# Performance work log

Hardware: AMD Instinct MI355X
Metric: run time of the kernel (lower is better)

The kernel has to match this reference:

```python
import jax, jax.numpy as jnp
import numpy as np

EPS = 1e-12  # torch F.normalize eps
RBF_SCALE = 10.0


def _l2norm(x, axis=-1):
    n = jnp.sqrt(jnp.sum(x * x, axis=axis, keepdims=True))
    return x / jnp.maximum(n, EPS)


def setup_inputs() -> dict:
    key = jax.random.key(0)
    k1, k2, k3 = jax.random.split(key, 3)
    N, D, C = 32768, 1024, 2048
    inp = jax.random.normal(k1, (N, D), dtype=jnp.float32)
    pos = jax.random.normal(k2, (C, D), dtype=jnp.float32)
    # offset is initialized to zeros in torch; use small random values so the
    # output is non-trivial for kernel correctness testing.
    offset = 0.01 * jax.random.normal(k3, (C, D), dtype=jnp.float32)
    return {"inp": inp, "pos": pos, "offset": offset}


def reference(inp, pos, offset):
    a = _l2norm(inp)                       # [N, D]
    b = _l2norm(pos)                       # [C, D]
    dist = 1.0 - jnp.einsum('nd,cd->nc', a, b)   # [N, C] cosine distance
    w = jnp.exp(-RBF_SCALE * dist)               # RBF cluster weights
    # The torch for-loop  out += offset[i] * dist[:, i, None]  is a GEMM:
    out = inp + jnp.einsum('nc,cd->nd', w, offset)
    out = _l2norm(out)
    offset_reg = jnp.sum(offset * offset)
    return (out, offset_reg)
```

## Files before the change

kernel.cpp:

```cpp
#include <hip/hip_runtime.h>

typedef float  f32x4  __attribute__((ext_vector_type(4)));
typedef float  f32x16 __attribute__((ext_vector_type(16)));
typedef int    i32x4  __attribute__((ext_vector_type(4)));
typedef int    i32x8  __attribute__((ext_vector_type(8)));

__device__ __forceinline__ unsigned int f2e4m3(float x){
    union{float f; unsigned u;} v; v.f = x;
    unsigned s = (v.u >> 24) & 0x80u;
    float ax = fabsf(x);
    if (ax > 448.0f) ax = 448.0f;
    if (ax < 0.015625f){
        int d = (int)__builtin_rintf(ax * 512.0f);
        return s | (unsigned)d;
    }
    v.f = ax;
    unsigned u = v.u + 0x7ffffu + ((v.u >> 20) & 1u);
    unsigned E = (u >> 23) - 120u;
    unsigned M = (u >> 20) & 7u;
    return s | (E << 3) | M;
}

__device__ __forceinline__ unsigned int pk4(float x0, float x1, float x2, float x3){
#if __has_builtin(__builtin_amdgcn_cvt_pk_fp8_f32)
    int u = __builtin_amdgcn_cvt_pk_fp8_f32(x0, x1, 0, false);
    u     = __builtin_amdgcn_cvt_pk_fp8_f32(x2, x3, u, true);
    return (unsigned)u;
#else
    return f2e4m3(x0) | (f2e4m3(x1) << 8) | (f2e4m3(x2) << 16) | (f2e4m3(x3) << 24);
#endif
}

__device__ __forceinline__ i32x8 ld_frag(const char* p0, const char* p1){
    i32x4 lo = *(const i32x4*)p0;
    i32x4 hi = *(const i32x4*)p1;
    return __builtin_shufflevector(lo, hi, 0,1,2,3,4,5,6,7);
}


__global__ __launch_bounds__(256) void norm_rows_fp8(const float* __restrict__ in,
                                                     unsigned char* __restrict__ out){
    const int row = blockIdx.x;
    const int t   = threadIdx.x;
    f32x4 x = ((const f32x4*)(in + (size_t)row * 1024))[t];
    float ss = x[0]*x[0] + x[1]*x[1] + x[2]*x[2] + x[3]*x[3];
    #pragma unroll
    for (int o = 32; o > 0; o >>= 1) ss += __shfl_xor(ss, o);
    __shared__ float red[4];
    if ((t & 63) == 0) red[t >> 6] = ss;
    __syncthreads();
    float tot = red[0] + red[1] + red[2] + red[3];
    float inv = 16.0f / fmaxf(sqrtf(tot), 1e-12f);
    unsigned u = pk4(x[0]*inv, x[1]*inv, x[2]*inv, x[3]*inv);
    size_t addr = ((size_t)(row >> 5) * 16 + (t >> 4)) * 2048
                + (size_t)((t >> 3) & 1) * 1024
                + (size_t)(row & 31) * 32 + ((4 * t) & 31);
    *(unsigned int*)(out + addr) = u;
}

__global__ __launch_bounds__(256) void norm_rows_f32(float* __restrict__ buf){
    const int row = blockIdx.x;
    const int t   = threadIdx.x;
    f32x4* p = (f32x4*)(buf + (size_t)row * 1024);
    f32x4 x = p[t];
    float ss = x[0]*x[0] + x[1]*x[1] + x[2]*x[2] + x[3]*x[3];
    #pragma unroll
    for (int o = 32; o > 0; o >>= 1) ss += __shfl_xor(ss, o);
    __shared__ float red[4];
    if ((t & 63) == 0) red[t >> 6] = ss;
    __syncthreads();
    float tot = red[0] + red[1] + red[2] + red[3];
    float inv = 1.0f / fmaxf(sqrtf(tot), 1e-12f);
    p[t] = x * inv;
}

__global__ __launch_bounds__(256) void transpose_off(const float* __restrict__ off,
                                                     unsigned char* __restrict__ offt,
                                                     float* __restrict__ reg_out){
    __shared__ unsigned char t_lds[64][68];
    const int t  = threadIdx.x;
    const int c0 = blockIdx.x * 64;
    const int d0 = blockIdx.y * 64;
    float ss = 0.f;
    #pragma unroll
    for (int p = 0; p < 4; ++p){
        int c  = p * 16 + (t >> 4);
        int dq = t & 15;
        f32x4 v = *(const f32x4*)(off + (size_t)(c0 + c) * 1024 + d0 + dq * 4);
        ss += v[0]*v[0] + v[1]*v[1] + v[2]*v[2] + v[3]*v[3];
        unsigned u = pk4(v[0]*64.0f, v[1]*64.0f, v[2]*64.0f, v[3]*64.0f);
        #pragma unroll
        for (int j = 0; j < 4; ++j) t_lds[dq * 4 + j][c] = (unsigned char)(u >> (8*j));
    }
    __syncthreads();
    #pragma unroll
    for (int i = 0; i < 4; ++i){
        int byte_o = (t + 256 * i) * 4;
        int fs  = byte_o >> 11;
        int rem = byte_o & 2047;
        int dl  = fs * 32 + ((rem >> 5) & 31);
        int cl  = ((rem >> 10) & 1) * 32 + (rem & 31);
        unsigned int v = *(const unsigned int*)&t_lds[dl][cl];
        size_t f = (size_t)((d0 >> 5) + fs);
        *(unsigned int*)(offt + (f * 32 + (c0 >> 6)) * 2048 + rem) = v;
    }
    #pragma unroll
    for (int o = 32; o > 0; o >>= 1) ss += __shfl_xor(ss, o);
    __shared__ float red[4];
    if ((t & 63) == 0) red[t >> 6] = ss;
    __syncthreads();
    if (t == 0) atomicAdd(reg_out, red[0] + red[1] + red[2] + red[3]);
}

template<int EPI, int SA, int SB, int NT>
__global__ __launch_bounds__(256, 2)
void gemm_fl(const unsigned char* __restrict__ A,
             const unsigned char* __restrict__ B,
             unsigned char* __restrict__ Wout, int wNT,
             const float* __restrict__ Cadd,
             float* __restrict__ Fout, int ldo)
{
    const int tid = threadIdx.x;

    int bx = blockIdx.x, by = blockIdx.y;
    {
        const int gx = gridDim.x, gy = gridDim.y;
        const int nwg = gx * gy;
        if ((nwg & 7) == 0){
            const int lid = bx + gx * by;
            const int q   = nwg >> 3;
            const int n   = (lid & 7) * q + (lid >> 3);
            const int sh  = 31 - __clz(gy);
            bx = n >> sh;
            by = n & (gy - 1);
        }
    }
    const int m0  = bx * 256;
    const int n0  = by * 128;
    const int wid = tid >> 6, lane = tid & 63;
    const int wr  = wid >> 1, wc = wid & 1;
    const int l31 = lane & 31, hg = lane >> 5;

    const char* pA[4];
    const char* pB[2];
    #pragma unroll
    for (int m = 0; m < 4; ++m)
        pA[m] = (const char*)A
              + ((size_t)((m0 + wr * 128 + m * 32) >> 5) * NT) * 2048 + lane * 32;
    #pragma unroll
    for (int n = 0; n < 2; ++n)
        pB[n] = (const char*)B
              + ((size_t)((n0 + wc * 64 + n * 32) >> 5) * NT) * 2048 + lane * 32;

    f32x16 acc[4][2] = {};
    i32x8 a0[4], b0[2], a1[4], b1[2];

    #pragma unroll
    for (int m = 0; m < 4; ++m) a0[m] = ld_frag(pA[m], pA[m] + 16);
    #pragma unroll
    for (int n = 0; n < 2; ++n) b0[n] = ld_frag(pB[n], pB[n] + 16);

#define MFMA8(av, bv) { __builtin_amdgcn_s_setprio(1); \
    _Pragma("unroll") for (int mi = 0; mi < 4; ++mi) \
    _Pragma("unroll") for (int ni = 0; ni < 2; ++ni) \
        acc[mi][ni] = __builtin_amdgcn_mfma_scale_f32_32x32x64_f8f6f4( \
            av[mi], bv[ni], acc[mi][ni], 0, 0, 0, SA, 0, SB); \
    __builtin_amdgcn_s_setprio(0); }

    #pragma unroll 1
    for (int t = 0; t < NT; t += 2){
        const size_t o1 = (size_t)(t + 1) * 2048;
        #pragma unroll
        for (int m = 0; m < 4; ++m) a1[m] = ld_frag(pA[m] + o1, pA[m] + o1 + 16);
        #pragma unroll
        for (int n = 0; n < 2; ++n) b1[n] = ld_frag(pB[n] + o1, pB[n] + o1 + 16);
        MFMA8(a0, b0);
        const size_t o2 = (size_t)(t + 2 < NT ? t + 2 : NT - 1) * 2048;
        #pragma unroll
        for (int m = 0; m < 4; ++m) a0[m] = ld_frag(pA[m] + o2, pA[m] + o2 + 16);
        #pragma unroll
        for (int n = 0; n < 2; ++n) b0[n] = ld_frag(pB[n] + o2, pB[n] + o2 + 16);
        MFMA8(a1, b1);
    }
#undef MFMA8

    asm volatile("s_nop 7\n\ts_nop 7");

    if (EPI == 1){
        const int tq = (n0 + wc * 64) >> 6;
        #pragma unroll
        for (int m = 0; m < 4; ++m){
            const size_t fW = (size_t)((m0 + wr * 128 + m * 32) >> 5);
            #pragma unroll
            for (int n = 0; n < 2; ++n){
                unsigned char* base = Wout + (fW * wNT + tq) * 2048
                                    + (size_t)n * 1024 + l31;
                #pragma unroll
                for (int q = 0; q < 4; ++q){
                    float w0 = exp2f(fmaf(14.4269504f, acc[m][n][4*q+0], -4.4269504f));
                    float w1 = exp2f(fmaf(14.4269504f, acc[m][n][4*q+1], -4.4269504f));
                    float w2 = exp2f(fmaf(14.4269504f, acc[m][n][4*q+2], -4.4269504f));
                    float w3 = exp2f(fmaf(14.4269504f, acc[m][n][4*q+3], -4.4269504f));
                    unsigned u = pk4(w0, w1, w2, w3);
                    unsigned char* p = base + (size_t)(8 * q + 4 * hg) * 32;
                    p[0]  = (unsigned char)u;
                    p[32] = (unsigned char)(u >> 8);
                    p[64] = (unsigned char)(u >> 16);
                    p[96] = (unsigned char)(u >> 24);
                }
            }
        }
    } else {
        #pragma unroll
        for (int m = 0; m < 4; ++m){
            #pragma unroll
            for (int n = 0; n < 2; ++n){
                const int grb = m0 + wr * 128 + m * 32;
                const int gc  = n0 + wc * 64 + n * 32 + l31;
                #pragma unroll
                for (int r = 0; r < 16; ++r){
                    const int row = (r & 3) + 8 * (r >> 2) + 4 * hg;
                    Fout[(size_t)(grb + row) * ldo + gc] =
                        Cadd[(size_t)(grb + row) * ldo + gc] + acc[m][n][r];
                }
            }
        }
    }
}

extern "C" void kernel_launch(void* const* d_in, const int* in_sizes, int n_in,
                              void* d_out, int out_size, void* d_ws, size_t ws_size,
                              hipStream_t stream)
{
    (void)n_in; (void)out_size;
    const float* inp = (const float*)d_in[0];
    const float* pos = (const float*)d_in[1];
    const float* off = (const float*)d_in[2];
    float* out = (float*)d_out;

    const int D = 1024, C = 2048;
    const int N = in_sizes[0] / D;

    unsigned char* b_fp8 = (unsigned char*)d_ws;
    unsigned char* offt  = b_fp8 + (size_t)C * D;
    unsigned char* a_fp8 = offt + (size_t)D * C;
    size_t fixed = (size_t)C * D * 2;
    size_t avail = ws_size > fixed ? ws_size - fixed : 0;
    int Mc = 256;
    for (int cand = N; cand >= 256; cand >>= 1){
        if ((size_t)cand * (size_t)(D + C) <= avail){ Mc = cand; break; }
    }
    if (Mc > N) Mc = N;
    unsigned char* w_buf = a_fp8 + (size_t)Mc * D;

    float* reg_out = out + (size_t)N * D;
    hipMemsetAsync(reg_out, 0, sizeof(float), stream);

    transpose_off<<<dim3(C / 64, D / 64), 256, 0, stream>>>(off, offt, reg_out);
    norm_rows_fp8<<<C, 256, 0, stream>>>(pos, b_fp8);

    for (int r0 = 0; r0 < N; r0 += Mc){
        norm_rows_fp8<<<Mc, 256, 0, stream>>>(inp + (size_t)r0 * D, a_fp8);
        gemm_fl<1,123,123,16><<<dim3(Mc / 256, C / 128), 256, 0, stream>>>(
            a_fp8, b_fp8, w_buf, C / 64, nullptr, nullptr, 0);
        gemm_fl<2,117,121,32><<<dim3(Mc / 256, D / 128), 256, 0, stream>>>(
            w_buf, offt, nullptr, 0, inp + (size_t)r0 * D, out + (size_t)r0 * D, D);
    }
    norm_rows_f32<<<N, 256, 0, stream>>>(out);
}
```

Baseline: 279.4 us.

## Stage A tiles through LDS with async global-to-LDS loads in 256x256 blocks

Replaces the register-only fp8 GEMM with a hybrid kernel that streams the row-major A operand into a triple-buffered, swizzled LDS ring using global_load_lds. B fragments are still loaded straight from global in the pre-tiled layout. The block tile grows to 256x256 with 512 threads, so A data is shared across more waves and fewer blocks re-read it. The activations and the weight buffer now use a plain row-major layout. This adds a barrier on every K step and 48KB of LDS per block, and the W epilogue still does scattered byte stores.

```diff
diff --git a/kernel.cpp b/kernel.cpp
--- a/kernel.cpp
+++ b/kernel.cpp
@@ -4,6 +4,9 @@
 typedef float  f32x16 __attribute__((ext_vector_type(16)));
 typedef int    i32x4  __attribute__((ext_vector_type(4)));
 typedef int    i32x8  __attribute__((ext_vector_type(8)));
+
+#define AS1 __attribute__((address_space(1)))
+#define AS3 __attribute__((address_space(3)))
 
 __device__ __forceinline__ unsigned int f2e4m3(float x){
     union{float f; unsigned u;} v; v.f = x;
@@ -31,15 +34,38 @@
 #endif
 }
 
+__device__ __forceinline__ void gload16(const unsigned char* g, const char* l){
+    __builtin_amdgcn_global_load_lds((const AS1 void*)g, (AS3 void*)l, 16, 0, 0);
+}
+
 __device__ __forceinline__ i32x8 ld_frag(const char* p0, const char* p1){
     i32x4 lo = *(const i32x4*)p0;
     i32x4 hi = *(const i32x4*)p1;
     return __builtin_shufflevector(lo, hi, 0,1,2,3,4,5,6,7);
 }
 
-
-__global__ __launch_bounds__(256) void norm_rows_fp8(const float* __restrict__ in,
-                                                     unsigned char* __restrict__ out){
+#define GBAR() do{ asm volatile("" ::: "memory"); __builtin_amdgcn_s_barrier(); \
+                   asm volatile("" ::: "memory"); }while(0)
+#define VMW(N)  asm volatile("s_waitcnt vmcnt(" #N ")" ::: "memory")
+
+__global__ __launch_bounds__(256) void norm_rows_fp8_rm(const float* __restrict__ in,
+                                                        unsigned int* __restrict__ out){
+    const int row = blockIdx.x;
+    const int t   = threadIdx.x;
+    f32x4 x = ((const f32x4*)(in + (size_t)row * 1024))[t];
+    float ss = x[0]*x[0] + x[1]*x[1] + x[2]*x[2] + x[3]*x[3];
+    #pragma unroll
+    for (int o = 32; o > 0; o >>= 1) ss += __shfl_xor(ss, o);
+    __shared__ float red[4];
+    if ((t & 63) == 0) red[t >> 6] = ss;
+    __syncthreads();
+    float tot = red[0] + red[1] + red[2] + red[3];
+    float inv = 16.0f / fmaxf(sqrtf(tot), 1e-12f);
+    out[(size_t)row * 256 + t] = pk4(x[0]*inv, x[1]*inv, x[2]*inv, x[3]*inv);
+}
+
+__global__ __launch_bounds__(256) void norm_rows_fp8_fl(const float* __restrict__ in,
+                                                        unsigned char* __restrict__ out){
     const int row = blockIdx.x;
     const int t   = threadIdx.x;
     f32x4 x = ((const f32x4*)(in + (size_t)row * 1024))[t];
@@ -112,14 +138,15 @@
     if (t == 0) atomicAdd(reg_out, red[0] + red[1] + red[2] + red[3]);
 }
 
-template<int EPI, int SA, int SB, int NT>
-__global__ __launch_bounds__(256, 2)
-void gemm_fl(const unsigned char* __restrict__ A,
-             const unsigned char* __restrict__ B,
-             unsigned char* __restrict__ Wout, int wNT,
-             const float* __restrict__ Cadd,
-             float* __restrict__ Fout, int ldo)
+template<int EPI, int SA, int SB>
+__global__ __launch_bounds__(512, 2)
+void gemm_hyb(const unsigned char* __restrict__ A, int lda,
+              const unsigned char* __restrict__ B,
+              int K,
+              unsigned char* __restrict__ Wout, int ldw,
+              const float* __restrict__ Cadd, float* __restrict__ Fout, int ldo)
 {
+    extern __shared__ char smem[];
     const int tid = threadIdx.x;
 
     int bx = blockIdx.x, by = blockIdx.y;
@@ -136,87 +163,109 @@
         }
     }
     const int m0  = bx * 256;
-    const int n0  = by * 128;
+    const int n0  = by * 256;
     const int wid = tid >> 6, lane = tid & 63;
-    const int wr  = wid >> 1, wc = wid & 1;
+    const int wr  = wid >> 2, wc = wid & 3;
     const int l31 = lane & 31, hg = lane >> 5;
-
-    const char* pA[4];
+    const int NT  = K >> 6;
+
+    const int srow = tid >> 2;
+    const int sg   = (tid & 3) ^ ((tid >> 3) & 3);
+    const unsigned char* sA = A + (size_t)(m0 + srow) * lda + sg * 16;
+    const int lp = tid * 16;
+    auto stgA = [&](int buf, int ke){
+        char* wb = smem + buf * 16384;
+        gload16(sA + ke, wb + lp);
+        gload16(sA + (size_t)128 * lda + ke, wb + 8192 + lp);
+    };
+
+    int aoff[4][2];
+    #pragma unroll
+    for (int m = 0; m < 4; ++m){
+        int row = wr * 128 + m * 32 + l31;
+        int sw  = (row >> 1) & 3;
+        aoff[m][0] = row * 64 + (((hg << 1) | 0) ^ sw) * 16;
+        aoff[m][1] = row * 64 + (((hg << 1) | 1) ^ sw) * 16;
+    }
+
     const char* pB[2];
-    #pragma unroll
-    for (int m = 0; m < 4; ++m)
-        pA[m] = (const char*)A
-              + ((size_t)((m0 + wr * 128 + m * 32) >> 5) * NT) * 2048 + lane * 32;
     #pragma unroll
     for (int n = 0; n < 2; ++n)
         pB[n] = (const char*)B
-              + ((size_t)((n0 + wc * 64 + n * 32) >> 5) * NT) * 2048 + lane * 32;
+              + (size_t)(((n0 + wc * 64 + n * 32) >> 5) * NT) * 2048 + lane * 32;
 
     f32x16 acc[4][2] = {};
-    i32x8 a0[4], b0[2], a1[4], b1[2];
-
-    #pragma unroll
-    for (int m = 0; m < 4; ++m) a0[m] = ld_frag(pA[m], pA[m] + 16);
-    #pragma unroll
-    for (int n = 0; n < 2; ++n) b0[n] = ld_frag(pB[n], pB[n] + 16);
-
-#define MFMA8(av, bv) { __builtin_amdgcn_s_setprio(1); \
+    i32x8 fa[4], bcur[2], bnxt[2];
+
+#define MFMA8(bv) { __builtin_amdgcn_s_setprio(1); \
     _Pragma("unroll") for (int mi = 0; mi < 4; ++mi) \
     _Pragma("unroll") for (int ni = 0; ni < 2; ++ni) \
         acc[mi][ni] = __builtin_amdgcn_mfma_scale_f32_32x32x64_f8f6f4( \
-            av[mi], bv[ni], acc[mi][ni], 0, 0, 0, SA, 0, SB); \
+            fa[mi], bv[ni], acc[mi][ni], 0, 0, 0, SA, 0, SB); \
     __builtin_amdgcn_s_setprio(0); }
 
+    stgA(0, 0);
+    stgA(1, 64);
+    #pragma unroll
+    for (int n = 0; n < 2; ++n) bcur[n] = ld_frag(pB[n], pB[n] + 16);
+    VMW(6);
+    GBAR();
+
+    int bufc = 0;
     #pragma unroll 1
-    for (int t = 0; t < NT; t += 2){
-        const size_t o1 = (size_t)(t + 1) * 2048;
+    for (int t = 0; t < NT - 1; ++t){
+        const char* rb = smem + bufc * 16384;
         #pragma unroll
-        for (int m = 0; m < 4; ++m) a1[m] = ld_frag(pA[m] + o1, pA[m] + o1 + 16);
+        for (int m = 0; m < 4; ++m)
+            fa[m] = ld_frag(rb + aoff[m][0], rb + aoff[m][1]);
+        {
+            const size_t o = (size_t)(t + 1) * 2048;
+            #pragma unroll
+            for (int n = 0; n < 2; ++n) bnxt[n] = ld_frag(pB[n] + o, pB[n] + o + 16);
+        }
+        MFMA8(bcur);
+        VMW(4);
+        GBAR();
+        if (t + 2 < NT){
+            int bs = bufc + 2; if (bs >= 3) bs -= 3;
+            stgA(bs, (t + 2) * 64);
+        }
+        bcur[0] = bnxt[0]; bcur[1] = bnxt[1];
+        ++bufc; if (bufc == 3) bufc = 0;
+    }
+    {
+        const char* rb = smem + bufc * 16384;
         #pragma unroll
-        for (int n = 0; n < 2; ++n) b1[n] = ld_frag(pB[n] + o1, pB[n] + o1 + 16);
-        MFMA8(a0, b0);
-        const size_t o2 = (size_t)(t + 2 < NT ? t + 2 : NT - 1) * 2048;
+        for (int m = 0; m < 4; ++m)
+            fa[m] = ld_frag(rb + aoff[m][0], rb + aoff[m][1]);
+        MFMA8(bcur);
+    }
+#undef MFMA8
+
+    asm volatile("s_nop 7\n\ts_nop 7");
+
+    #pragma unroll
+    for (int m = 0; m < 4; ++m){
         #pragma unroll
-        for (int m = 0; m < 4; ++m) a0[m] = ld_frag(pA[m] + o2, pA[m] + o2 + 16);
-        #pragma unroll
-        for (int n = 0; n < 2; ++n) b0[n] = ld_frag(pB[n] + o2, pB[n] + o2 + 16);
-        MFMA8(a1, b1);
-    }
-#undef MFMA8
-
-    asm volatile("s_nop 7\n\ts_nop 7");
-
-    if (EPI == 1){
-        const int tq = (n0 + wc * 64) >> 6;
-        #pragma unroll
-        for (int m = 0; m < 4; ++m){
-            const size_t fW = (size_t)((m0 + wr * 128 + m * 32) >> 5);
-            #pragma unroll
-            for (int n = 0; n < 2; ++n){
-                unsigned char* base = Wout + (fW * wNT + tq) * 2048
-                                    + (size_t)n * 1024 + l31;
+        for (int n = 0; n < 2; ++n){
+            const int grb = m0 + wr * 128 + m * 32;
+            const int gc  = n0 + wc * 64  + n * 32 + l31;
+            if (EPI == 1){
                 #pragma unroll
                 for (int q = 0; q < 4; ++q){
+                    const int row0 = grb + 8 * q + 4 * hg;
                     float w0 = exp2f(fmaf(14.4269504f, acc[m][n][4*q+0], -4.4269504f));
                     float w1 = exp2f(fmaf(14.4269504f, acc[m][n][4*q+1], -4.4269504f));
                     float w2 = exp2f(fmaf(14.4269504f, acc[m][n][4*q+2], -4.4269504f));
                     float w3 = exp2f(fmaf(14.4269504f, acc[m][n][4*q+3], -4.4269504f));
                     unsigned u = pk4(w0, w1, w2, w3);
-                    unsigned char* p = base + (size_t)(8 * q + 4 * hg) * 32;
-                    p[0]  = (unsigned char)u;
-                    p[32] = (unsigned char)(u >> 8);
-                    p[64] = (unsigned char)(u >> 16);
-                    p[96] = (unsigned char)(u >> 24);
+                    unsigned char* p = Wout + (size_t)row0 * ldw + gc;
+                    p[0]                = (unsigned char)u;
+                    p[(size_t)ldw]      = (unsigned char)(u >> 8);
+                    p[(size_t)ldw * 2]  = (unsigned char)(u >> 16);
+                    p[(size_t)ldw * 3]  = (unsigned char)(u >> 24);
                 }
-            }
-        }
-    } else {
-        #pragma unroll
-        for (int m = 0; m < 4; ++m){
-            #pragma unroll
-            for (int n = 0; n < 2; ++n){
-                const int grb = m0 + wr * 128 + m * 32;
-                const int gc  = n0 + wc * 64 + n * 32 + l31;
+            } else {
                 #pragma unroll
                 for (int r = 0; r < 16; ++r){
                     const int row = (r & 3) + 8 * (r >> 2) + 4 * hg;
@@ -253,18 +302,23 @@
     if (Mc > N) Mc = N;
     unsigned char* w_buf = a_fp8 + (size_t)Mc * D;
 
+    hipFuncSetAttribute(reinterpret_cast<const void*>(&gemm_hyb<1,123,123>),
+                        hipFuncAttributeMaxDynamicSharedMemorySize, 49152);
+    hipFuncSetAttribute(reinterpret_cast<const void*>(&gemm_hyb<2,117,121>),
+                        hipFuncAttributeMaxDynamicSharedMemorySize, 49152);
+
     float* reg_out = out + (size_t)N * D;
     hipMemsetAsync(reg_out, 0, sizeof(float), stream);
 
     transpose_off<<<dim3(C / 64, D / 64), 256, 0, stream>>>(off, offt, reg_out);
-    norm_rows_fp8<<<C, 256, 0, stream>>>(pos, b_fp8);
+    norm_rows_fp8_fl<<<C, 256, 0, stream>>>(pos, b_fp8);
 
     for (int r0 = 0; r0 < N; r0 += Mc){
-        norm_rows_fp8<<<Mc, 256, 0, stream>>>(inp + (size_t)r0 * D, a_fp8);
-        gemm_fl<1,123,123,16><<<dim3(Mc / 256, C / 128), 256, 0, stream>>>(
-            a_fp8, b_fp8, w_buf, C / 64, nullptr, nullptr, 0);
-        gemm_fl<2,117,121,32><<<dim3(Mc / 256, D / 128), 256, 0, stream>>>(
-            w_buf, offt, nullptr, 0, inp + (size_t)r0 * D, out + (size_t)r0 * D, D);
+        norm_rows_fp8_rm<<<Mc, 256, 0, stream>>>(inp + (size_t)r0 * D, (unsigned int*)a_fp8);
+        gemm_hyb<1,123,123><<<dim3(Mc / 256, C / 256), 512, 49152, stream>>>(
+            a_fp8, D, b_fp8, D, w_buf, C, nullptr, nullptr, 0);
+        gemm_hyb<2,117,121><<<dim3(Mc / 256, D / 256), 512, 49152, stream>>>(
+            w_buf, C, offt, C, nullptr, 0, inp + (size_t)r0 * D, out + (size_t)r0 * D, D);
     }
     norm_rows_f32<<<N, 256, 0, stream>>>(out);
 }
```

New measurement: 289.2 us. +3.5%, slower.
